# Kernel tuning notes

Measured on AMD Instinct MI355X. Metric: run time of the kernel, lower is better.

Reference implementation:

```python
import jax, jax.numpy as jnp
import numpy as np
from jax import lax

B, CIN, CH, HW, K = 256, 256, 256, 16, 3


def setup_inputs() -> dict:
    key = jax.random.key(0)
    ks = jax.random.split(key, 9)
    s = 0.05
    return {
        "x": jax.random.normal(ks[0], (B, CIN, HW, HW), dtype=jnp.float32),
        "h": jax.random.normal(ks[1], (B, CH, HW, HW), dtype=jnp.float32),
        "c": jax.random.normal(ks[2], (B, CH, HW, HW), dtype=jnp.float32),
        # stacked x-branch conv weights for gates [i, f, c, o]; no bias (matches torch code)
        "Wx": jax.random.normal(ks[3], (4 * CH, CIN, K, K), dtype=jnp.float32) * s,
        # stacked h-branch conv weights for gates [i, f, c, o]; with bias
        "Wh": jax.random.normal(ks[4], (4 * CH, CH, K, K), dtype=jnp.float32) * s,
        "bh": jax.random.normal(ks[5], (4 * CH,), dtype=jnp.float32) * s,
        # peephole params (torch inits them to zeros; use small randn to exercise the math)
        "Wci": jax.random.normal(ks[6], (1, CH, HW, HW), dtype=jnp.float32) * s,
        "Wcf": jax.random.normal(ks[7], (1, CH, HW, HW), dtype=jnp.float32) * s,
        "Wco": jax.random.normal(ks[8], (1, CH, HW, HW), dtype=jnp.float32) * s,
    }


def _conv(x, w):
    # same-padding 2D conv, NCHW/OIHW
    return lax.conv_general_dilated(
        x, w, window_strides=(1, 1), padding="SAME",
        dimension_numbers=("NCHW", "OIHW", "NCHW"))


def reference(x, h, c, Wx, Wh, bh, Wci, Wcf, Wco):
    gx = _conv(x, Wx)                                   # [B, 4*CH, H, W]
    gh = _conv(h, Wh) + bh[None, :, None, None]         # [B, 4*CH, H, W]
    xi, xf, xc, xo = jnp.split(gx, 4, axis=1)
    hi, hf, hc, ho = jnp.split(gh, 4, axis=1)
    i_t = jax.nn.sigmoid(xi + hi + Wci * c)
    f_t = jax.nn.sigmoid(xf + hf + Wcf * c)
    c_t = f_t * c + i_t * jnp.tanh(xc + hc)
    o_t = jax.nn.sigmoid(xo + ho + Wco * c_t)
    h_t = o_t * jnp.tanh(c_t)
    return (h_t, c_t)
```

## Files before the change

### kernel.cpp

```cpp
#include <hip/hip_runtime.h>


typedef __bf16 bf16x8 __attribute__((ext_vector_type(8)));
typedef float f32x16 __attribute__((ext_vector_type(16)));

#define PLANE_B  20736u
#define XH_BYTES (4096u * PLANE_B)
#define OUT_HALF 16777216u

__device__ inline void gload_lds16(const void* g, void* l) {
    __builtin_amdgcn_global_load_lds(
        (const __attribute__((address_space(1))) void*)g,
        (__attribute__((address_space(3))) void*)l, 16, 0, 0);
}

__global__ __launch_bounds__(256) void xh_transform(
    const float* __restrict__ x, const float* __restrict__ hh,
    unsigned char* __restrict__ xh)
{
    int blk = blockIdx.x;
    int b = blk >> 4, ibk = blk & 15;
    const float* src = (ibk < 8) ? (x  + ((size_t)(b*256 + ibk*32)) * 256)
                                 : (hh + ((size_t)(b*256 + (ibk-8)*32)) * 256);
    int t = threadIdx.x;
    uint32_t w[16];
#pragma unroll
    for (int i = 0; i < 16; ++i) {
        __bf16 lo = (__bf16)src[(size_t)(2*i  )*256 + t];
        __bf16 hi = (__bf16)src[(size_t)(2*i+1)*256 + t];
        w[i] = (uint32_t)__builtin_bit_cast(unsigned short, lo)
             | ((uint32_t)__builtin_bit_cast(unsigned short, hi) << 16);
    }
    unsigned char* plane = xh + (size_t)blk * PLANE_B;
    int p = ((t >> 4) + 1)*18 + (t & 15) + 1;
    uint32_t key  = (uint32_t)(p & 7) << 4;
    uint32_t base = (uint32_t)p * 64u;
#pragma unroll
    for (int k = 0; k < 4; ++k)
        *(uint4*)(plane + ((base + 16u*k) ^ key)) =
            uint4{w[4*k], w[4*k+1], w[4*k+2], w[4*k+3]};
    if (t < 68) {
        int pb;
        if      (t < 18) pb = t;
        else if (t < 36) pb = 17*18 + (t - 18);
        else if (t < 52) pb = (t - 35)*18;
        else             pb = (t - 51)*18 + 17;
        uint32_t kb = (uint32_t)(pb & 7) << 4;
        uint32_t bb = (uint32_t)pb * 64u;
        uint4 z{0u,0u,0u,0u};
#pragma unroll
        for (int k = 0; k < 4; ++k)
            *(uint4*)(plane + ((bb + 16u*k) ^ kb)) = z;
    }
}

__global__ __launch_bounds__(256) void w_transform(
    const float* __restrict__ Wx, const float* __restrict__ Wh,
    __bf16* __restrict__ Wt)
{
    int idx  = blockIdx.x * 256 + threadIdx.x;
    int lane = idx & 63;
    int chunk = idx >> 6;
    int half  = chunk & 1;
    int icblk = (chunk >> 1) & 15;
    int fg    = (chunk >> 5) & 3;
    int cb    = (chunk >> 7) & 7;
    int pos   = chunk >> 10;
    int row = lane & 31, hl = lane >> 5;
    int gate = row & 3, ch8 = row >> 2;
    int oc  = gate*256 + cb*32 + fg*8 + ch8;
    int ic0 = icblk*32 + half*16 + hl*8;
    bf16x8 v;
#pragma unroll
    for (int j = 0; j < 8; ++j) {
        int ic = ic0 + j;
        float w = (ic < 256) ? Wx[((size_t)oc*256 + ic      )*9 + pos]
                             : Wh[((size_t)oc*256 + (ic-256))*9 + pos];
        v[j] = (__bf16)w;
    }
    *(bf16x8*)(Wt + (size_t)chunk*512 + (size_t)lane*8) = v;
}

__global__ __launch_bounds__(256, 2) void convlstm_main(
    const unsigned char* __restrict__ xh, const __bf16* __restrict__ Wt,
    const float* __restrict__ bh,  const float* __restrict__ cin,
    const float* __restrict__ Wci, const float* __restrict__ Wcf,
    const float* __restrict__ Wco, float* __restrict__ out)
{
    int bid = blockIdx.x;
    int cb  = bid & 7;
    int nh  = (bid >> 3) & 1;
    int b   = bid >> 4;
    int tid = threadIdx.x;
    int lane = tid & 63, wv = tid >> 6;
    int l31 = lane & 31, hl = lane >> 5;

    __shared__ __align__(16) unsigned char lds[2][24576];

    f32x16 acc[2][2];
#pragma unroll
    for (int f = 0; f < 2; ++f) {
        int fg = nh*2 + f;
        f32x16 v;
#pragma unroll
        for (int r = 0; r < 16; ++r) {
            int gate = r & 3, q = r >> 2;
            v[r] = bh[gate*256 + cb*32 + fg*8 + 2*q + hl];
        }
        acc[0][f] = v; acc[1][f] = v;
    }

    const unsigned char* planes = xh + (size_t)b * (16u * PLANE_B);

#pragma unroll
    for (int k = 0; k < 6; ++k)
        gload_lds16(planes + (size_t)(wv*6 + k)*1024u + (size_t)lane*16u,
                    &lds[0][(wv*6 + k)*1024 + lane*16]);

    int m0 = wv*64 + l31,       m1 = wv*64 + 32 + l31;
    int pbase0 = (m0 >> 4)*18 + (m0 & 15);
    int pbase1 = (m1 >> 4)*18 + (m1 & 15);

    const __bf16* wlane = Wt + (size_t)lane * 8;
    auto achunk = [&](int ibk, int ph, int f) -> size_t {
        int pos = ph >> 1, half = ph & 1, fg = nh*2 + f;
        return ((size_t)((pos*8 + cb)*4 + fg))*32 + (size_t)(ibk*2 + half);
    };

    __syncthreads();

    bf16x8 A[2][2];
    A[0][0] = *(const bf16x8*)(wlane + achunk(0, 0, 0)*512);
    A[0][1] = *(const bf16x8*)(wlane + achunk(0, 0, 1)*512);

    for (int ibk = 0; ibk < 16; ++ibk) {
        const int cur = ibk & 1;
        if (ibk < 15) {
            const unsigned char* np = planes + (size_t)(ibk+1) * PLANE_B;
#pragma unroll
            for (int k = 0; k < 6; ++k)
                gload_lds16(np + (size_t)(wv*6 + k)*1024u + (size_t)lane*16u,
                            &lds[cur ^ 1][(wv*6 + k)*1024 + lane*16]);
        }
        const unsigned char* rb = lds[cur];
#pragma unroll
        for (int ph = 0; ph < 18; ++ph) {
            {
                int nib = (ph < 17) ? ibk : ((ibk < 15) ? ibk + 1 : ibk);
                int nph = (ph < 17) ? ph + 1 : 0;
                A[(ph+1)&1][0] = *(const bf16x8*)(wlane + achunk(nib, nph, 0)*512);
                A[(ph+1)&1][1] = *(const bf16x8*)(wlane + achunk(nib, nph, 1)*512);
            }
            const int pos = ph >> 1, half = ph & 1;
            const int dp = (pos/3)*18 + (pos%3);
            const uint32_t kofs = (uint32_t)(half*32 + hl*16);
            bf16x8 B0, B1;
            {
                int p = pbase0 + dp;
                uint32_t byte = ((uint32_t)p*64u + kofs) ^ ((uint32_t)(p&7) << 4);
                B0 = *(const bf16x8*)(rb + byte);
            }
            {
                int p = pbase1 + dp;
                uint32_t byte = ((uint32_t)p*64u + kofs) ^ ((uint32_t)(p&7) << 4);
                B1 = *(const bf16x8*)(rb + byte);
            }
            __builtin_amdgcn_s_setprio(1);
            acc[0][0] = __builtin_amdgcn_mfma_f32_32x32x16_bf16(A[ph&1][0], B0, acc[0][0], 0, 0, 0);
            acc[0][1] = __builtin_amdgcn_mfma_f32_32x32x16_bf16(A[ph&1][1], B0, acc[0][1], 0, 0, 0);
            acc[1][0] = __builtin_amdgcn_mfma_f32_32x32x16_bf16(A[ph&1][0], B1, acc[1][0], 0, 0, 0);
            acc[1][1] = __builtin_amdgcn_mfma_f32_32x32x16_bf16(A[ph&1][1], B1, acc[1][1], 0, 0, 0);
            __builtin_amdgcn_s_setprio(0);
        }
        __syncthreads();
    }

    float* outh = out;
    float* outc = out + (size_t)OUT_HALF;
    const size_t bOff = (size_t)b * (256*256);
#pragma unroll
    for (int mf = 0; mf < 2; ++mf) {
        int m = wv*64 + mf*32 + l31;
#pragma unroll
        for (int f = 0; f < 2; ++f) {
            int fg = nh*2 + f;
#pragma unroll
            for (int q = 0; q < 4; ++q) {
                int ch = cb*32 + fg*8 + 2*q + hl;
                size_t pidx = (size_t)ch*256 + (size_t)m;
                size_t idx  = bOff + pidx;
                float cv = cin[idx];
                float pi = acc[mf][f][4*q+0];
                float pf = acc[mf][f][4*q+1];
                float pc = acc[mf][f][4*q+2];
                float po = acc[mf][f][4*q+3];
                float it = 1.f/(1.f + __expf(-(pi + Wci[pidx]*cv)));
                float ft = 1.f/(1.f + __expf(-(pf + Wcf[pidx]*cv)));
                float tc = 1.f - 2.f/(1.f + __expf(2.f*pc));
                float ct = ft*cv + it*tc;
                float ot = 1.f/(1.f + __expf(-(po + Wco[pidx]*ct)));
                float th = 1.f - 2.f/(1.f + __expf(2.f*ct));
                outh[idx] = ot*th;
                outc[idx] = ct;
            }
        }
    }
}

extern "C" void kernel_launch(void* const* d_in, const int* in_sizes, int n_in,
                              void* d_out, int out_size, void* d_ws, size_t ws_size,
                              hipStream_t stream)
{
    const float* x   = (const float*)d_in[0];
    const float* h   = (const float*)d_in[1];
    const float* c   = (const float*)d_in[2];
    const float* Wx  = (const float*)d_in[3];
    const float* Wh  = (const float*)d_in[4];
    const float* bh  = (const float*)d_in[5];
    const float* Wci = (const float*)d_in[6];
    const float* Wcf = (const float*)d_in[7];
    const float* Wco = (const float*)d_in[8];
    float* out = (float*)d_out;

    unsigned char* xh = (unsigned char*)d_ws;
    __bf16* Wt = (__bf16*)(xh + (size_t)XH_BYTES + 4096);

    hipLaunchKernelGGL(xh_transform, dim3(4096), dim3(256), 0, stream, x, h, xh);
    hipLaunchKernelGGL(w_transform,  dim3(2304), dim3(256), 0, stream, Wx, Wh, Wt);
    hipLaunchKernelGGL(convlstm_main, dim3(4096), dim3(256), 0, stream,
                       xh, Wt, bh, c, Wci, Wcf, Wco, out);
}
```

Before: 651.1 us.

## Prefetch LDS B fragments one phase ahead and raise occupancy to three blocks

Double-buffers the B operand reads from LDS so the next phase's fragments load while the current MFMAs run, hiding LDS latency. Also raises the launch-bounds minimum blocks per CU from two to three, increasing occupancy and cutting the per-thread register budget. This risks register spills given the large accumulator and fragment register footprint.

```diff
diff --git a/kernel.cpp b/kernel.cpp
--- a/kernel.cpp
+++ b/kernel.cpp
@@ -81,7 +81,7 @@
     *(bf16x8*)(Wt + (size_t)chunk*512 + (size_t)lane*8) = v;
 }
 
-__global__ __launch_bounds__(256, 2) void convlstm_main(
+__global__ __launch_bounds__(256, 3) void convlstm_main(
     const unsigned char* __restrict__ xh, const __bf16* __restrict__ Wt,
     const float* __restrict__ bh,  const float* __restrict__ cin,
     const float* __restrict__ Wci, const float* __restrict__ Wcf,
@@ -120,12 +120,20 @@
     int m0 = wv*64 + l31,       m1 = wv*64 + 32 + l31;
     int pbase0 = (m0 >> 4)*18 + (m0 & 15);
     int pbase1 = (m1 >> 4)*18 + (m1 & 15);
+    const uint32_t kbase = (uint32_t)(hl*16);
 
     const __bf16* wlane = Wt + (size_t)lane * 8;
     auto achunk = [&](int ibk, int ph, int f) -> size_t {
         int pos = ph >> 1, half = ph & 1, fg = nh*2 + f;
         return ((size_t)((pos*8 + cb)*4 + fg))*32 + (size_t)(ibk*2 + half);
     };
+    auto bread = [&](const unsigned char* rb, int pbase, int ph) -> bf16x8 {
+        int pos = ph >> 1, half = ph & 1;
+        int p = pbase + (pos/3)*18 + (pos%3);
+        uint32_t byte = ((uint32_t)p*64u + kbase + (uint32_t)(half*32))
+                        ^ (((uint32_t)(p & 7)) << 4);
+        return *(const bf16x8*)(rb + byte);
+    };
 
     __syncthreads();
 
@@ -143,6 +151,11 @@
                             &lds[cur ^ 1][(wv*6 + k)*1024 + lane*16]);
         }
         const unsigned char* rb = lds[cur];
+
+        bf16x8 Bb[2][2];
+        Bb[0][0] = bread(rb, pbase0, 0);
+        Bb[0][1] = bread(rb, pbase1, 0);
+
 #pragma unroll
         for (int ph = 0; ph < 18; ++ph) {
             {
@@ -151,25 +164,15 @@
                 A[(ph+1)&1][0] = *(const bf16x8*)(wlane + achunk(nib, nph, 0)*512);
                 A[(ph+1)&1][1] = *(const bf16x8*)(wlane + achunk(nib, nph, 1)*512);
             }
-            const int pos = ph >> 1, half = ph & 1;
-            const int dp = (pos/3)*18 + (pos%3);
-            const uint32_t kofs = (uint32_t)(half*32 + hl*16);
-            bf16x8 B0, B1;
-            {
-                int p = pbase0 + dp;
-                uint32_t byte = ((uint32_t)p*64u + kofs) ^ ((uint32_t)(p&7) << 4);
-                B0 = *(const bf16x8*)(rb + byte);
-            }
-            {
-                int p = pbase1 + dp;
-                uint32_t byte = ((uint32_t)p*64u + kofs) ^ ((uint32_t)(p&7) << 4);
-                B1 = *(const bf16x8*)(rb + byte);
+            if (ph < 17) {
+                Bb[(ph+1)&1][0] = bread(rb, pbase0, ph+1);
+                Bb[(ph+1)&1][1] = bread(rb, pbase1, ph+1);
             }
             __builtin_amdgcn_s_setprio(1);
-            acc[0][0] = __builtin_amdgcn_mfma_f32_32x32x16_bf16(A[ph&1][0], B0, acc[0][0], 0, 0, 0);
-            acc[0][1] = __builtin_amdgcn_mfma_f32_32x32x16_bf16(A[ph&1][1], B0, acc[0][1], 0, 0, 0);
-            acc[1][0] = __builtin_amdgcn_mfma_f32_32x32x16_bf16(A[ph&1][0], B1, acc[1][0], 0, 0, 0);
-            acc[1][1] = __builtin_amdgcn_mfma_f32_32x32x16_bf16(A[ph&1][1], B1, acc[1][1], 0, 0, 0);
+            acc[0][0] = __builtin_amdgcn_mfma_f32_32x32x16_bf16(A[ph&1][0], Bb[ph&1][0], acc[0][0], 0, 0, 0);
+            acc[0][1] = __builtin_amdgcn_mfma_f32_32x32x16_bf16(A[ph&1][1], Bb[ph&1][0], acc[0][1], 0, 0, 0);
+            acc[1][0] = __builtin_amdgcn_mfma_f32_32x32x16_bf16(A[ph&1][0], Bb[ph&1][1], acc[1][0], 0, 0, 0);
+            acc[1][1] = __builtin_amdgcn_mfma_f32_32x32x16_bf16(A[ph&1][1], Bb[ph&1][1], acc[1][1], 0, 0, 0);
             __builtin_amdgcn_s_setprio(0);
         }
         __syncthreads();
```

After: 640.2 us. About the same (-1.7%).

## Drop LDS staging; stream A and B fragments directly from global

Applied to the files above, without the earlier changes.

Removes the LDS double buffer and its barriers. Each wave now loads its input-plane B fragments straight from global or L2 into registers, using a three-deep register pipeline for both A and B. The weight layout is reordered so each (cb, nh) block reads its A fragments as one contiguous stream advancing 2 KB per step, and the XOR swizzle on the planes is dropped. The aim is to cut LDS traffic and synchronisation stalls, at the cost of more global/L2 load traffic and latency that the MFMA loop must hide.

```diff
diff --git a/kernel.cpp b/kernel.cpp
--- a/kernel.cpp
+++ b/kernel.cpp
@@ -5,14 +5,8 @@
 typedef float f32x16 __attribute__((ext_vector_type(16)));
 
 #define PLANE_B  20736u
-#define XH_BYTES (4096u * PLANE_B)
+#define WT_BYTES 9441280u
 #define OUT_HALF 16777216u
-
-__device__ inline void gload_lds16(const void* g, void* l) {
-    __builtin_amdgcn_global_load_lds(
-        (const __attribute__((address_space(1))) void*)g,
-        (__attribute__((address_space(3))) void*)l, 16, 0, 0);
-}
 
 __global__ __launch_bounds__(256) void xh_transform(
     const float* __restrict__ x, const float* __restrict__ hh,
@@ -33,24 +27,20 @@
     }
     unsigned char* plane = xh + (size_t)blk * PLANE_B;
     int p = ((t >> 4) + 1)*18 + (t & 15) + 1;
-    uint32_t key  = (uint32_t)(p & 7) << 4;
-    uint32_t base = (uint32_t)p * 64u;
-#pragma unroll
-    for (int k = 0; k < 4; ++k)
-        *(uint4*)(plane + ((base + 16u*k) ^ key)) =
-            uint4{w[4*k], w[4*k+1], w[4*k+2], w[4*k+3]};
+    uint4* dst = (uint4*)(plane + (uint32_t)p*64u);
+    dst[0] = uint4{w[0],  w[1],  w[2],  w[3]};
+    dst[1] = uint4{w[4],  w[5],  w[6],  w[7]};
+    dst[2] = uint4{w[8],  w[9],  w[10], w[11]};
+    dst[3] = uint4{w[12], w[13], w[14], w[15]};
     if (t < 68) {
         int pb;
         if      (t < 18) pb = t;
         else if (t < 36) pb = 17*18 + (t - 18);
         else if (t < 52) pb = (t - 35)*18;
         else             pb = (t - 51)*18 + 17;
-        uint32_t kb = (uint32_t)(pb & 7) << 4;
-        uint32_t bb = (uint32_t)pb * 64u;
         uint4 z{0u,0u,0u,0u};
-#pragma unroll
-        for (int k = 0; k < 4; ++k)
-            *(uint4*)(plane + ((bb + 16u*k) ^ kb)) = z;
+        uint4* zd = (uint4*)(plane + (uint32_t)pb*64u);
+        zd[0] = z; zd[1] = z; zd[2] = z; zd[3] = z;
     }
 }
 
@@ -61,15 +51,17 @@
     int idx  = blockIdx.x * 256 + threadIdx.x;
     int lane = idx & 63;
     int chunk = idx >> 6;
-    int half  = chunk & 1;
-    int icblk = (chunk >> 1) & 15;
-    int fg    = (chunk >> 5) & 3;
-    int cb    = (chunk >> 7) & 7;
-    int pos   = chunk >> 10;
+    int f     = chunk & 1;
+    int half  = (chunk >> 1) & 1;
+    int pos   = (chunk >> 2) % 9;
+    int rest  = (chunk >> 2) / 9;
+    int ibk   = rest & 15;
+    int cbnh  = rest >> 4;
+    int nh = cbnh & 1, cb = cbnh >> 1;
     int row = lane & 31, hl = lane >> 5;
     int gate = row & 3, ch8 = row >> 2;
-    int oc  = gate*256 + cb*32 + fg*8 + ch8;
-    int ic0 = icblk*32 + half*16 + hl*8;
+    int oc  = gate*256 + cb*32 + (nh*2 + f)*8 + ch8;
+    int ic0 = ibk*32 + half*16 + hl*8;
     bf16x8 v;
 #pragma unroll
     for (int j = 0; j < 8; ++j) {
@@ -82,7 +74,7 @@
 }
 
 __global__ __launch_bounds__(256, 2) void convlstm_main(
-    const unsigned char* __restrict__ xh, const __bf16* __restrict__ Wt,
+    const unsigned char* __restrict__ xh, const unsigned char* __restrict__ Wtb,
     const float* __restrict__ bh,  const float* __restrict__ cin,
     const float* __restrict__ Wci, const float* __restrict__ Wcf,
     const float* __restrict__ Wco, float* __restrict__ out)
@@ -95,8 +87,6 @@
     int lane = tid & 63, wv = tid >> 6;
     int l31 = lane & 31, hl = lane >> 5;
 
-    __shared__ __align__(16) unsigned char lds[2][24576];
-
     f32x16 acc[2][2];
 #pragma unroll
     for (int f = 0; f < 2; ++f) {
@@ -110,69 +100,50 @@
         acc[0][f] = v; acc[1][f] = v;
     }
 
-    const unsigned char* planes = xh + (size_t)b * (16u * PLANE_B);
-
-#pragma unroll
-    for (int k = 0; k < 6; ++k)
-        gload_lds16(planes + (size_t)(wv*6 + k)*1024u + (size_t)lane*16u,
-                    &lds[0][(wv*6 + k)*1024 + lane*16]);
-
-    int m0 = wv*64 + l31,       m1 = wv*64 + 32 + l31;
-    int pbase0 = (m0 >> 4)*18 + (m0 & 15);
-    int pbase1 = (m1 >> 4)*18 + (m1 & 15);
-
-    const __bf16* wlane = Wt + (size_t)lane * 8;
-    auto achunk = [&](int ibk, int ph, int f) -> size_t {
-        int pos = ph >> 1, half = ph & 1, fg = nh*2 + f;
-        return ((size_t)((pos*8 + cb)*4 + fg))*32 + (size_t)(ibk*2 + half);
-    };
-
-    __syncthreads();
-
-    bf16x8 A[2][2];
-    A[0][0] = *(const bf16x8*)(wlane + achunk(0, 0, 0)*512);
-    A[0][1] = *(const bf16x8*)(wlane + achunk(0, 0, 1)*512);
+    const unsigned char* planeB = xh  + (size_t)b * (16u * PLANE_B);
+    const unsigned char* wbase  = Wtb + (size_t)(cb*2 + nh) * 589824u;
+
+    int m0 = wv*64 + l31, m1 = m0 + 32;
+    uint32_t voffB0 = (uint32_t)(((m0 >> 4)*18 + (m0 & 15))*64 + hl*16);
+    uint32_t voffB1 = (uint32_t)(((m1 >> 4)*18 + (m1 & 15))*64 + hl*16);
+    uint32_t voffA  = (uint32_t)(lane*16);
+
+    bf16x8 A[3][2], Bb[3][2];
+    A[0][0] = *(const bf16x8*)(wbase + voffA + 0);
+    A[0][1] = *(const bf16x8*)(wbase + voffA + 1024);
+    A[1][0] = *(const bf16x8*)(wbase + voffA + 2048);
+    A[1][1] = *(const bf16x8*)(wbase + voffA + 3072);
+    Bb[0][0] = *(const bf16x8*)(planeB + voffB0 + 0);
+    Bb[0][1] = *(const bf16x8*)(planeB + voffB1 + 0);
+    Bb[1][0] = *(const bf16x8*)(planeB + voffB0 + 32);
+    Bb[1][1] = *(const bf16x8*)(planeB + voffB1 + 32);
 
     for (int ibk = 0; ibk < 16; ++ibk) {
-        const int cur = ibk & 1;
-        if (ibk < 15) {
-            const unsigned char* np = planes + (size_t)(ibk+1) * PLANE_B;
-#pragma unroll
-            for (int k = 0; k < 6; ++k)
-                gload_lds16(np + (size_t)(wv*6 + k)*1024u + (size_t)lane*16u,
-                            &lds[cur ^ 1][(wv*6 + k)*1024 + lane*16]);
-        }
-        const unsigned char* rb = lds[cur];
-#pragma unroll
-        for (int ph = 0; ph < 18; ++ph) {
-            {
-                int nib = (ph < 17) ? ibk : ((ibk < 15) ? ibk + 1 : ibk);
-                int nph = (ph < 17) ? ph + 1 : 0;
-                A[(ph+1)&1][0] = *(const bf16x8*)(wlane + achunk(nib, nph, 0)*512);
-                A[(ph+1)&1][1] = *(const bf16x8*)(wlane + achunk(nib, nph, 1)*512);
-            }
-            const int pos = ph >> 1, half = ph & 1;
-            const int dp = (pos/3)*18 + (pos%3);
-            const uint32_t kofs = (uint32_t)(half*32 + hl*16);
-            bf16x8 B0, B1;
-            {
-                int p = pbase0 + dp;
-                uint32_t byte = ((uint32_t)p*64u + kofs) ^ ((uint32_t)(p&7) << 4);
-                B0 = *(const bf16x8*)(rb + byte);
+#pragma unroll
+        for (int p = 0; p < 18; ++p) {
+            voffA += 2048u;
+            if (p == 16 && ibk < 15) {
+                voffB0 += PLANE_B;
+                voffB1 += PLANE_B;
             }
             {
-                int p = pbase1 + dp;
-                uint32_t byte = ((uint32_t)p*64u + kofs) ^ ((uint32_t)(p&7) << 4);
-                B1 = *(const bf16x8*)(rb + byte);
+                const int tp = p + 2;
+                const int tl = (tp < 18) ? tp : tp - 18;
+                const uint32_t blit =
+                    (uint32_t)(((((tl >> 1) / 3)*18 + ((tl >> 1) % 3))*64)
+                               + (tl & 1)*32);
+                A[(p+2)%3][0] = *(const bf16x8*)(wbase + voffA + 2048u);
+                A[(p+2)%3][1] = *(const bf16x8*)(wbase + voffA + 3072u);
+                Bb[(p+2)%3][0] = *(const bf16x8*)(planeB + voffB0 + blit);
+                Bb[(p+2)%3][1] = *(const bf16x8*)(planeB + voffB1 + blit);
             }
             __builtin_amdgcn_s_setprio(1);
-            acc[0][0] = __builtin_amdgcn_mfma_f32_32x32x16_bf16(A[ph&1][0], B0, acc[0][0], 0, 0, 0);
-            acc[0][1] = __builtin_amdgcn_mfma_f32_32x32x16_bf16(A[ph&1][1], B0, acc[0][1], 0, 0, 0);
-            acc[1][0] = __builtin_amdgcn_mfma_f32_32x32x16_bf16(A[ph&1][0], B1, acc[1][0], 0, 0, 0);
-            acc[1][1] = __builtin_amdgcn_mfma_f32_32x32x16_bf16(A[ph&1][1], B1, acc[1][1], 0, 0, 0);
+            acc[0][0] = __builtin_amdgcn_mfma_f32_32x32x16_bf16(A[p%3][0], Bb[p%3][0], acc[0][0], 0, 0, 0);
+            acc[0][1] = __builtin_amdgcn_mfma_f32_32x32x16_bf16(A[p%3][1], Bb[p%3][0], acc[0][1], 0, 0, 0);
+            acc[1][0] = __builtin_amdgcn_mfma_f32_32x32x16_bf16(A[p%3][0], Bb[p%3][1], acc[1][0], 0, 0, 0);
+            acc[1][1] = __builtin_amdgcn_mfma_f32_32x32x16_bf16(A[p%3][1], Bb[p%3][1], acc[1][1], 0, 0, 0);
             __builtin_amdgcn_s_setprio(0);
         }
-        __syncthreads();
     }
 
     float* outh = out;
@@ -222,11 +193,12 @@
     const float* Wco = (const float*)d_in[8];
     float* out = (float*)d_out;
 
-    unsigned char* xh = (unsigned char*)d_ws;
-    __bf16* Wt = (__bf16*)(xh + (size_t)XH_BYTES + 4096);
+    unsigned char* wtb = (unsigned char*)d_ws;
+    unsigned char* xh  = wtb + (size_t)WT_BYTES;
 
     hipLaunchKernelGGL(xh_transform, dim3(4096), dim3(256), 0, stream, x, h, xh);
-    hipLaunchKernelGGL(w_transform,  dim3(2304), dim3(256), 0, stream, Wx, Wh, Wt);
+    hipLaunchKernelGGL(w_transform,  dim3(2304), dim3(256), 0, stream,
+                       Wx, Wh, (__bf16*)wtb);
     hipLaunchKernelGGL(convlstm_main, dim3(4096), dim3(256), 0, stream,
-                       xh, Wt, bh, c, Wci, Wcf, Wco, out);
-}
+                       xh, wtb, bh, c, Wci, Wcf, Wco, out);
+}
```

After: 946.0 us. 1.45x slower.
